# Optimization experiments

Measured on AMD Instinct MI355X. Metric: run time of the kernel, lower is better.

Reference implementation:

```python
import jax, jax.numpy as jnp
import numpy as np

B, C, H, W = 8, 384, 32, 32
KEYS, HEADS, U = 16, 4, 1
VS = C // HEADS
N = H * W
BN_EPS = 1e-5


def setup_inputs() -> dict:
    key = jax.random.key(0)
    ks = jax.random.split(key, 8)
    x = jax.random.normal(ks[0], (B, C, H, W), dtype=jnp.float32)
    # 1x1 convs (spectral-normalized in torch; SN only rescales the weight,
    # so a plain weight matrix computes the same functional form)
    Wq = jax.random.normal(ks[1], (KEYS * HEADS, C), dtype=jnp.float32) * 0.02
    Wk = jax.random.normal(ks[2], (KEYS * U, C), dtype=jnp.float32) * 0.02
    Wv = jax.random.normal(ks[3], (VS * U, C), dtype=jnp.float32) * 0.02
    # BatchNorm affine params (torch code xavier-inits weight, zeros bias)
    gamma_q = jax.random.normal(ks[4], (KEYS * HEADS,), dtype=jnp.float32)
    beta_q = jnp.zeros((KEYS * HEADS,), dtype=jnp.float32)
    gamma_v = jax.random.normal(ks[5], (VS * U,), dtype=jnp.float32)
    beta_v = jnp.zeros((VS * U,), dtype=jnp.float32)
    pos_emb = jax.random.normal(ks[6], (N, N, KEYS, U), dtype=jnp.float32)
    return {"x": x, "Wq": Wq, "Wk": Wk, "Wv": Wv,
            "gamma_q": gamma_q, "beta_q": beta_q,
            "gamma_v": gamma_v, "beta_v": beta_v,
            "pos_emb": pos_emb}


def _bn(z, gamma, beta):
    # z: (B, Ch, N); BatchNorm2d in training mode: biased batch stats over (B, N)
    mean = jnp.mean(z, axis=(0, 2), keepdims=True)
    var = jnp.var(z, axis=(0, 2), keepdims=True)
    zn = (z - mean) * jax.lax.rsqrt(var + BN_EPS)
    return zn * gamma[None, :, None] + beta[None, :, None]


def reference(x, Wq, Wk, Wv, gamma_q, beta_q, gamma_v, beta_v, pos_emb):
    xf = x.reshape(B, C, N)                       # 1x1 conv == per-pixel matmul
    q = jnp.einsum('oc,bcn->bon', Wq, xf)         # (B, KEYS*HEADS, N)
    k = jnp.einsum('oc,bcn->bon', Wk, xf)         # (B, KEYS*U, N)
    v = jnp.einsum('oc,bcn->bon', Wv, xf)         # (B, VS*U, N)
    q = _bn(q, gamma_q, beta_q)
    v = _bn(v, gamma_v, beta_v)
    q = q.reshape(B, HEADS, KEYS, N)
    k = k.reshape(B, U, KEYS, N)
    v = v.reshape(B, U, VS, N)
    k = jax.nn.softmax(k, axis=-1)
    lambdac = jnp.einsum('bukm,buvm->bkv', k, v)          # content lambda
    Yc = jnp.einsum('bhkn,bkv->bhvn', q, lambdac)
    lambdap = jnp.einsum('nmku,buvm->bnkv', pos_emb, v)   # position lambda (B,N,K,V)
    Yp = jnp.einsum('bhkn,bnkv->bhvn', q, lambdap)
    Y = (Yc + Yp).reshape(B, C, H, W)
    return Y
```

## Files before the change

kernel.cpp:

```cpp
#include <hip/hip_runtime.h>

typedef __attribute__((ext_vector_type(8))) short short8;
typedef __attribute__((ext_vector_type(16))) float floatx16;
typedef __attribute__((ext_vector_type(4))) float floatx4;
typedef unsigned short ushort16_t;
typedef unsigned int uint32;

#define BB 8
#define CC 384
#define NPIX 1024
#define TOTCH 176
#define BN_EPS 1e-5f

__device__ __forceinline__ ushort16_t f2bf(float x) {
    uint32 u = __float_as_uint(x);
    u += 0x7FFFu + ((u >> 16) & 1u);
    return (ushort16_t)(u >> 16);
}
__device__ __forceinline__ uint32 pk2(float a, float b) {
    uint32 ua = __float_as_uint(a); ua += 0x7FFFu + ((ua >> 16) & 1u);
    uint32 ub = __float_as_uint(b); ub += 0x7FFFu + ((ub >> 16) & 1u);
    return (ua >> 16) | (ub & 0xFFFF0000u);
}
__device__ __forceinline__ int div48(int x) {
    return (int)(((unsigned)x * 21846u) >> 20);
}
#define LGKM0_ONLY 0xC07F

__device__ __forceinline__ void gload8h(short8 &d, const ushort16_t* p) {
    asm volatile("global_load_dwordx4 %0, %1, off" : "=v"(d) : "v"(p));
}
__device__ __forceinline__ void gload4f(float4 &d, const float* p) {
    asm volatile("global_load_dwordx4 %0, %1, off" : "=v"(d) : "v"(p));
}


__global__ __launch_bounds__(256, 2) void k_wt(const float* __restrict__ Wq,
    const float* __restrict__ Wk, const float* __restrict__ Wv,
    ushort16_t* __restrict__ wbf)
{
    int bx = blockIdx.x, t = threadIdx.x;
    #pragma unroll
    for (int jj = 0; jj < 9; ++jj) {
        int idx8 = (bx * 9 + jj) * 256 + t;
        int row = div48(idx8);
        int g   = idx8 - row * 48;
        float4 f0, f1;
        if (row < 176) {
            const float* src;
            if (row < 64)       src = Wq + (size_t)row * CC;
            else if (row < 80)  src = Wk + (size_t)(row - 64) * CC;
            else                src = Wv + (size_t)(row - 80) * CC;
            f0 = *(const float4*)(src + g * 8);
            f1 = *(const float4*)(src + g * 8 + 4);
        } else {
            f0.x = f0.y = f0.z = f0.w = 0.f;
            f1 = f0;
        }
        uint4 w;
        w.x = pk2(f0.x, f0.y); w.y = pk2(f0.z, f0.w);
        w.z = pk2(f1.x, f1.y); w.w = pk2(f1.z, f1.w);
        *(uint4*)&wbf[(size_t)row * CC + g * 8] = w;
    }
}

__global__ __launch_bounds__(256, 2) void k_proj(const float* __restrict__ x,
    const ushort16_t* __restrict__ wbf, float* __restrict__ qkv)
{
    __shared__ __align__(16) ushort16_t XT[32 * 392];
    int bx = blockIdx.x, t = threadIdx.x;
    int b = bx >> 5, nbase = (bx & 31) * 32;
    const float* xb = x + (size_t)b * (CC * NPIX) + nbase;
    #pragma unroll
    for (int j = 0; j < 12; ++j) {
        int idx = t + 256 * j;
        int c = idx >> 3, ng = idx & 7;
        float4 f = *(const float4*)(xb + (size_t)c * NPIX + ng * 4);
        int col = ng * 4;
        XT[(col + 0) * 392 + c] = f2bf(f.x);
        XT[(col + 1) * 392 + c] = f2bf(f.y);
        XT[(col + 2) * 392 + c] = f2bf(f.z);
        XT[(col + 3) * 392 + c] = f2bf(f.w);
    }
    __syncthreads();

    int wave = t >> 6, lane = t & 63;
    int ct = wave & 1;
    int rs = wave >> 1;
    int col1 = lane & 15, kq = lane >> 4;
    const ushort16_t* bbase = &XT[(ct * 16 + col1) * 392 + kq * 8];
    int n = nbase + ct * 16 + col1;

    for (int r = rs; r < 11; r += 2) {
        int r0 = r * 16;
        const ushort16_t* ap = wbf + (size_t)(r0 + col1) * CC + kq * 8;
        floatx4 acc = {0.f, 0.f, 0.f, 0.f};
        short8 a0 = *(const short8*)ap;
        short8 b0 = *(const short8*)bbase;
        #pragma unroll
        for (int k = 1; k < 12; ++k) {
            short8 a1 = *(const short8*)(ap + k * 32);
            short8 b1 = *(const short8*)(bbase + k * 32);
            acc = __builtin_amdgcn_mfma_f32_16x16x32_bf16(a0, b0, acc, 0, 0, 0);
            a0 = a1; b0 = b1;
        }
        acc = __builtin_amdgcn_mfma_f32_16x16x32_bf16(a0, b0, acc, 0, 0, 0);
        #pragma unroll
        for (int rr = 0; rr < 4; ++rr) {
            int ch = r0 + kq * 4 + rr;
            qkv[((size_t)b * TOTCH + ch) * NPIX + n] = acc[rr];
        }
    }
}

__global__ __launch_bounds__(256, 2) void k_bnsm(const float* __restrict__ qkv,
    const float* __restrict__ gq, const float* __restrict__ bq,
    const float* __restrict__ gv, const float* __restrict__ bv,
    float* __restrict__ sA, float* __restrict__ sB, float* __restrict__ ksm)
{
    int bx = blockIdx.x, tid = threadIdx.x;
    int wid = tid >> 6, lane = tid & 63;
    if (bx < 160) {
        int ch = bx;
        int row; float gamma, beta;
        if (ch < 64) { row = ch; gamma = gq[ch]; beta = bq[ch]; }
        else { int j = ch - 64; row = 80 + j; gamma = gv[j]; beta = bv[j]; }
        float s = 0.f, ss = 0.f;
        #pragma unroll
        for (int j = 0; j < 8; ++j) {
            int i4 = tid + 256 * j;
            int b = i4 >> 8, n4 = i4 & 255;
            float4 f = *(const float4*)(qkv + ((size_t)b * TOTCH + row) * NPIX
                                            + n4 * 4);
            s  += f.x + f.y + f.z + f.w;
            ss += f.x * f.x + f.y * f.y + f.z * f.z + f.w * f.w;
        }
        #pragma unroll
        for (int off = 32; off > 0; off >>= 1) {
            s  += __shfl_down(s, off);
            ss += __shfl_down(ss, off);
        }
        __shared__ float rs[4], rss[4];
        if (lane == 0) { rs[wid] = s; rss[wid] = ss; }
        __syncthreads();
        if (tid == 0) {
            float S  = rs[0] + rs[1] + rs[2] + rs[3];
            float SS = rss[0] + rss[1] + rss[2] + rss[3];
            float inv = 1.f / (BB * NPIX);
            float mean = S * inv;
            float var  = SS * inv - mean * mean;
            float a = gamma * rsqrtf(var + BN_EPS);
            sA[row] = a;
            sB[row] = beta - mean * a;
        }
    } else {
        int idx = bx - 160;
        int kc = idx & 15, b = idx >> 4;
        const float* rowp = qkv + ((size_t)b * TOTCH + 64 + kc) * NPIX;
        float4 v4 = *(const float4*)(rowp + tid * 4);
        float v[4] = {v4.x, v4.y, v4.z, v4.w};
        float mx = fmaxf(fmaxf(v[0], v[1]), fmaxf(v[2], v[3]));
        #pragma unroll
        for (int off = 32; off > 0; off >>= 1) mx = fmaxf(mx, __shfl_down(mx, off));
        __shared__ float sm[4], ssum[4];
        if (lane == 0) sm[wid] = mx;
        __syncthreads();
        mx = fmaxf(fmaxf(sm[0], sm[1]), fmaxf(sm[2], sm[3]));
        float e[4], s = 0.f;
        #pragma unroll
        for (int j = 0; j < 4; ++j) { e[j] = __expf(v[j] - mx); s += e[j]; }
        #pragma unroll
        for (int off = 32; off > 0; off >>= 1) s += __shfl_down(s, off);
        if (lane == 0) ssum[wid] = s;
        __syncthreads();
        float inv = 1.f / (ssum[0] + ssum[1] + ssum[2] + ssum[3]);
        float4 o;
        o.x = e[0] * inv; o.y = e[1] * inv; o.z = e[2] * inv; o.w = e[3] * inv;
        *(float4*)(ksm + ((size_t)b * 16 + kc) * NPIX + tid * 4) = o;
    }
}

__global__ __launch_bounds__(256, 2) void k_packlc(const float* __restrict__ qkv,
    const float* __restrict__ sA, const float* __restrict__ sB,
    const float* __restrict__ ksm,
    ushort16_t* __restrict__ qt_g, ushort16_t* __restrict__ vt_g,
    ushort16_t* __restrict__ lc_g)
{
    int bx = blockIdx.x, t = threadIdx.x;
    if (bx < 128) {
        int bh = t & 31, nn = (t >> 5) & 7;
        int n = bx * 8 + nn;
        int b = bh >> 2, h = bh & 3;
        float vals[16];
        #pragma unroll
        for (int k = 0; k < 16; ++k) {
            int ch = h * 16 + k;
            vals[k] = qkv[((size_t)b * TOTCH + ch) * NPIX + n] * sA[ch] + sB[ch];
        }
        uint4 w0, w1;
        w0.x = pk2(vals[0], vals[1]);  w0.y = pk2(vals[2], vals[3]);
        w0.z = pk2(vals[4], vals[5]);  w0.w = pk2(vals[6], vals[7]);
        w1.x = pk2(vals[8], vals[9]);  w1.y = pk2(vals[10], vals[11]);
        w1.z = pk2(vals[12], vals[13]); w1.w = pk2(vals[14], vals[15]);
        *(uint4*)&qt_g[(size_t)n * 512 + bh * 8]       = w0;
        *(uint4*)&qt_g[(size_t)n * 512 + 256 + bh * 8] = w1;
    } else if (bx < 512) {
        int gi = (bx - 128) * 256 + t;
        int m8 = gi & 127;
        int vg = (gi >> 7) % 96;
        int b  = gi / (96 * 128);
        int m  = m8 * 8;
        int row = 80 + vg;
        float a = sA[row], bb = sB[row];
        const float* p = qkv + ((size_t)b * TOTCH + row) * NPIX + m;
        float4 f0 = *(const float4*)p;
        float4 f1 = *(const float4*)(p + 4);
        uint4 w;
        w.x = pk2(f0.x * a + bb, f0.y * a + bb);
        w.y = pk2(f0.z * a + bb, f0.w * a + bb);
        w.z = pk2(f1.x * a + bb, f1.y * a + bb);
        w.w = pk2(f1.z * a + bb, f1.w * a + bb);
        int mt = m >> 5, mq = (m >> 3) & 3;
        int vhh = vg / 48, vtt = (vg % 48) >> 4, vl = vg & 15;
        size_t idx = ((((size_t)b * 32 + mt) * 2 + vhh) * 3 + vtt) * 512
                   + mq * 128 + vl * 8;
        *(uint4*)&vt_g[idx] = w;
    } else {
        int gi = bx - 512;
        int v = gi % 96, b = gi / 96;
        int row = 80 + v;
        float a = sA[row], bb = sB[row];
        const float* vp = qkv + ((size_t)b * TOTCH + row) * NPIX;
        const float* kp = ksm + (size_t)b * 16 * NPIX;
        float4 vv = *(const float4*)(vp + t * 4);
        float4 vhat;
        vhat.x = vv.x * a + bb; vhat.y = vv.y * a + bb;
        vhat.z = vv.z * a + bb; vhat.w = vv.w * a + bb;
        float acc[16];
        #pragma unroll
        for (int k = 0; k < 16; ++k) {
            float4 kk = *(const float4*)(kp + (size_t)k * NPIX + t * 4);
            acc[k] = kk.x * vhat.x + kk.y * vhat.y
                   + kk.z * vhat.z + kk.w * vhat.w;
        }
        #pragma unroll
        for (int k = 0; k < 16; ++k) {
            #pragma unroll
            for (int off = 32; off > 0; off >>= 1)
                acc[k] += __shfl_down(acc[k], off);
        }
        __shared__ float red[16][4];
        int wid = t >> 6, lane = t & 63;
        if (lane == 0) {
            #pragma unroll
            for (int k = 0; k < 16; ++k) red[k][wid] = acc[k];
        }
        __syncthreads();
        int vhh = v / 48, vtt = (v % 48) >> 4, vl = v & 15;
        size_t plane = ((size_t)(b * 2 + vhh) * 3 + vtt) * 512;
        if (t < 16) {
            int k = t;
            float val = red[k][0] + red[k][1] + red[k][2] + red[k][3];
            lc_g[plane + (k >> 3) * 128 + vl * 8 + (k & 7)] = f2bf(val);
        } else if (t < 18) {
            int mq = 2 + (t - 16);
            uint4 z; z.x = z.y = z.z = z.w = 0u;
            *(uint4*)&lc_g[plane + mq * 128 + vl * 8] = z;
        }
    }
}

__global__ __attribute__((amdgpu_flat_work_group_size(512, 512)))
__attribute__((amdgpu_waves_per_eu(2, 2)))
void k_main(const float* __restrict__ pos,
    const ushort16_t* __restrict__ qt_g, const ushort16_t* __restrict__ vt_g,
    const ushort16_t* __restrict__ lc_g, float* __restrict__ out)
{
    __shared__ __align__(16) ushort16_t S_s[2][8256];
    int tid  = threadIdx.x;
    int lane = tid & 63;
    int wave = tid >> 6;
    int n0 = blockIdx.x * 4;

    int col1 = lane & 31, half = lane >> 5;
    int nsub = wave & 3, mc0 = wave >> 2;

    int colw  = (col1 & 3) * 4 + nsub;
    int key3w = nsub + ((col1 & 1) << 2);
    int basew = (col1 >> 2) * 1032 + colw * 64 + half * 4;

    int b2 = wave;
    int c2 = lane & 15, kq = lane >> 4;
    int h2 = c2 >> 2, n2 = c2 & 3;
    int key3r = n2 + ((h2 & 1) << 2);
    int baser = b2 * 1032 + (h2 * 4 + n2) * 64;

    short8 qfr = *(const short8*)(qt_g + (size_t)(n0 + nsub) * 512
                                  + half * 256 + col1 * 8);

    floatx4 acc[6];
    #pragma unroll
    for (int vg = 0; vg < 6; ++vg) acc[vg] = floatx4{0.f, 0.f, 0.f, 0.f};

    floatx16 z16;
    #pragma unroll
    for (int i = 0; i < 16; ++i) z16[i] = 0.f;

    const float* pA = pos + ((size_t)(n0 + nsub) * 1024 + mc0 * 32 + col1) * 16
                    + half * 8;
    const ushort16_t* pV = vt_g + (size_t)b2 * 98304 + lane * 8;

    float4 pa[2], pb[2];
    gload4f(pa[0], pA);
    gload4f(pb[0], pA + 4);
    gload4f(pa[1], pA + 1024);
    gload4f(pb[1], pA + 1028);

    short8 vbuf[12];

    #pragma unroll
    for (int i = 0; i < 16; ++i) {
        const ushort16_t* pVi = pV + (size_t)i * 6144;
        #pragma unroll
        for (int vg = 0; vg < 6; ++vg)
            gload8h(vbuf[vg], pVi + vg * 512);
        #pragma unroll
        for (int vg = 0; vg < 6; ++vg)
            gload8h(vbuf[6 + vg], pVi + 3072 + vg * 512);

        if (i == 0) {
            asm volatile("s_waitcnt vmcnt(14)");
            __builtin_amdgcn_sched_barrier(0);
        }

        {
            float4 a0c = pa[i & 1], a1c = pb[i & 1];
            uint4 aw;
            aw.x = pk2(a0c.x, a0c.y); aw.y = pk2(a0c.z, a0c.w);
            aw.z = pk2(a1c.x, a1c.y); aw.w = pk2(a1c.z, a1c.w);
            short8 afr = *(short8*)&aw;
            floatx16 d = __builtin_amdgcn_mfma_f32_32x32x16_bf16(
                afr, qfr, z16, 0, 0, 0);
            ushort16_t* Sb = S_s[i & 1];
            #pragma unroll
            for (int q = 0; q < 4; ++q) {
                int slot = (mc0 * 4 + q) ^ key3w;
                uint2 wv;
                wv.x = pk2(d[q * 4 + 0], d[q * 4 + 1]);
                wv.y = pk2(d[q * 4 + 2], d[q * 4 + 3]);
                *(uint2*)&Sb[basew + slot * 8] = wv;
            }
        }

        if (i < 14) {
            const float* p = pA + (size_t)(i + 2) * 1024;
            gload4f(pa[i & 1], p);
            gload4f(pb[i & 1], p + 4);
        }

        __builtin_amdgcn_s_waitcnt(LGKM0_ONLY);
        __builtin_amdgcn_s_barrier();

        if (i < 14) asm volatile("s_waitcnt vmcnt(2)");
        else        asm volatile("s_waitcnt vmcnt(0)");
        __builtin_amdgcn_sched_barrier(0);

        {
            const ushort16_t* Sr = S_s[i & 1];
            short8 bs0 = *(const short8*)&Sr[baser + (kq ^ key3r) * 8];
            #pragma unroll
            for (int vg = 0; vg < 6; ++vg)
                acc[vg] = __builtin_amdgcn_mfma_f32_16x16x32_bf16(
                    vbuf[vg], bs0, acc[vg], 0, 0, 0);
            short8 bs1 = *(const short8*)&Sr[baser + ((4 + kq) ^ key3r) * 8];
            #pragma unroll
            for (int vg = 0; vg < 6; ++vg)
                acc[vg] = __builtin_amdgcn_mfma_f32_16x16x32_bf16(
                    vbuf[6 + vg], bs1, acc[vg], 0, 0, 0);
        }
    }

    {
        short8 bsq = {0, 0, 0, 0, 0, 0, 0, 0};
        if (kq < 2)
            bsq = *(const short8*)(qt_g + (size_t)(n0 + n2) * 512
                                   + kq * 256 + (b2 * 4 + h2) * 8);
        const ushort16_t* lsrc = lc_g + (size_t)b2 * 3072 + lane * 8;
        #pragma unroll
        for (int vg = 0; vg < 6; ++vg) {
            short8 lv = *(const short8*)(lsrc + vg * 512);
            acc[vg] = __builtin_amdgcn_mfma_f32_16x16x32_bf16(
                lv, bsq, acc[vg], 0, 0, 0);
        }
    }

    {
        #pragma unroll
        for (int vg = 0; vg < 6; ++vg) {
            int vbase = (vg / 3) * 48 + (vg % 3) * 16 + kq * 4;
            #pragma unroll
            for (int r = 0; r < 4; ++r) {
                int v = vbase + r;
                out[(size_t)(b2 * 384 + h2 * 96 + v) * 1024 + n0 + n2]
                    = acc[vg][r];
            }
        }
    }
}

extern "C" void kernel_launch(void* const* d_in, const int* in_sizes, int n_in,
                              void* d_out, int out_size, void* d_ws, size_t ws_size,
                              hipStream_t stream) {
    const float* x   = (const float*)d_in[0];
    const float* Wq  = (const float*)d_in[1];
    const float* Wk  = (const float*)d_in[2];
    const float* Wv  = (const float*)d_in[3];
    const float* gq  = (const float*)d_in[4];
    const float* bq  = (const float*)d_in[5];
    const float* gv  = (const float*)d_in[6];
    const float* bv  = (const float*)d_in[7];
    const float* pos = (const float*)d_in[8];
    float* out = (float*)d_out;
    float* ws  = (float*)d_ws;

    float* qkv = ws;
    float* sA  = ws + 1441792;
    float* sB  = ws + 1441968;
    float* ksm = ws + 1442144;
    ushort16_t* qt_g = (ushort16_t*)(ws + 1573216);
    ushort16_t* vt_g = (ushort16_t*)(ws + 1835360);
    ushort16_t* lc_g = (ushort16_t*)(ws + 2228576);
    ushort16_t* wbf  = (ushort16_t*)(ws + 3813728);

    k_wt<<<dim3(4), dim3(256), 0, stream>>>(Wq, Wk, Wv, wbf);
    k_proj<<<dim3(256), dim3(256), 0, stream>>>(x, wbf, qkv);
    k_bnsm<<<dim3(288), dim3(256), 0, stream>>>(qkv, gq, bq, gv, bv, sA, sB, ksm);
    k_packlc<<<dim3(1280), dim3(256), 0, stream>>>(qkv, sA, sB, ksm,
                                                   qt_g, vt_g, lc_g);
    k_main<<<dim3(256), dim3(512), 0, stream>>>(pos, qt_g, vt_g, lc_g, out);
}
```

Measured before the change: 169.5 us.

## Stream V tiles through LDS with global_load_lds double buffering

Replaces the per-iteration register loads of twelve V fragments with direct global-to-LDS loads into two LDS half-buffers. Each half is refilled as soon as its MFMAs have consumed it, and the vmcnt waits are re-tuned to match. The pos-embedding prefetch distance drops from two iterations to one. The aim is to cut VGPR pressure and overlap V streaming with compute, at the cost of about 96KB of extra LDS, extra LDS reads, and tighter hand-managed wait counts.

New measurement: 174.3 us. 2.8% more time.

```diff
diff --git a/kernel.cpp b/kernel.cpp
--- a/kernel.cpp
+++ b/kernel.cpp
@@ -27,9 +27,6 @@
 }
 #define LGKM0_ONLY 0xC07F
 
-__device__ __forceinline__ void gload8h(short8 &d, const ushort16_t* p) {
-    asm volatile("global_load_dwordx4 %0, %1, off" : "=v"(d) : "v"(p));
-}
 __device__ __forceinline__ void gload4f(float4 &d, const float* p) {
     asm volatile("global_load_dwordx4 %0, %1, off" : "=v"(d) : "v"(p));
 }
@@ -277,6 +274,7 @@
     const ushort16_t* __restrict__ lc_g, float* __restrict__ out)
 {
     __shared__ __align__(16) ushort16_t S_s[2][8256];
+    __shared__ __align__(16) ushort16_t Vv[2][24576];
     int tid  = threadIdx.x;
     int lane = tid & 63;
     int wave = tid >> 6;
@@ -308,30 +306,37 @@
 
     const float* pA = pos + ((size_t)(n0 + nsub) * 1024 + mc0 * 32 + col1) * 16
                     + half * 8;
-    const ushort16_t* pV = vt_g + (size_t)b2 * 98304 + lane * 8;
+    const ushort16_t* vsrc = vt_g + (size_t)wave * 98304 + lane * 8;
 
     float4 pa[2], pb[2];
+
+    __builtin_amdgcn_sched_barrier(0);
     gload4f(pa[0], pA);
     gload4f(pb[0], pA + 4);
-    gload4f(pa[1], pA + 1024);
-    gload4f(pb[1], pA + 1028);
-
-    short8 vbuf[12];
+    #pragma unroll
+    for (int vg = 0; vg < 6; ++vg)
+        __builtin_amdgcn_global_load_lds(
+            (const uint4*)(vsrc + vg * 512),
+            (uint4*)&Vv[0][wave * 3072 + vg * 512], 16, 0, 0);
+    #pragma unroll
+    for (int vg = 0; vg < 6; ++vg)
+        __builtin_amdgcn_global_load_lds(
+            (const uint4*)(vsrc + 3072 + vg * 512),
+            (uint4*)&Vv[1][wave * 3072 + vg * 512], 16, 0, 0);
+    __builtin_amdgcn_sched_barrier(0);
 
     #pragma unroll
     for (int i = 0; i < 16; ++i) {
-        const ushort16_t* pVi = pV + (size_t)i * 6144;
-        #pragma unroll
-        for (int vg = 0; vg < 6; ++vg)
-            gload8h(vbuf[vg], pVi + vg * 512);
-        #pragma unroll
-        for (int vg = 0; vg < 6; ++vg)
-            gload8h(vbuf[6 + vg], pVi + 3072 + vg * 512);
-
-        if (i == 0) {
+        if (i < 15) {
+            const float* p = pA + (size_t)(i + 1) * 1024;
+            __builtin_amdgcn_sched_barrier(0);
+            gload4f(pa[(i + 1) & 1], p);
+            gload4f(pb[(i + 1) & 1], p + 4);
             asm volatile("s_waitcnt vmcnt(14)");
-            __builtin_amdgcn_sched_barrier(0);
-        }
+        } else {
+            asm volatile("s_waitcnt vmcnt(12)");
+        }
+        __builtin_amdgcn_sched_barrier(0);
 
         {
             float4 a0c = pa[i & 1], a1c = pb[i & 1];
@@ -352,31 +357,55 @@
             }
         }
 
-        if (i < 14) {
-            const float* p = pA + (size_t)(i + 2) * 1024;
-            gload4f(pa[i & 1], p);
-            gload4f(pb[i & 1], p + 4);
-        }
-
         __builtin_amdgcn_s_waitcnt(LGKM0_ONLY);
         __builtin_amdgcn_s_barrier();
 
-        if (i < 14) asm volatile("s_waitcnt vmcnt(2)");
+        if (i < 15) asm volatile("s_waitcnt vmcnt(8)");
+        else        asm volatile("s_waitcnt vmcnt(6)");
+        __builtin_amdgcn_sched_barrier(0);
+        {
+            const ushort16_t* Sr = S_s[i & 1];
+            const ushort16_t* Vr0 = &Vv[0][b2 * 3072 + lane * 8];
+            short8 bs0 = *(const short8*)&Sr[baser + (kq ^ key3r) * 8];
+            #pragma unroll
+            for (int vg = 0; vg < 6; ++vg)
+                acc[vg] = __builtin_amdgcn_mfma_f32_16x16x32_bf16(
+                    *(const short8*)(Vr0 + vg * 512), bs0, acc[vg], 0, 0, 0);
+        }
+        if (i < 15) {
+            asm volatile("s_waitcnt lgkmcnt(0)");
+            __builtin_amdgcn_sched_barrier(0);
+            const ushort16_t* vs = vsrc + (size_t)(2 * i + 2) * 3072;
+            #pragma unroll
+            for (int vg = 0; vg < 6; ++vg)
+                __builtin_amdgcn_global_load_lds(
+                    (const uint4*)(vs + vg * 512),
+                    (uint4*)&Vv[0][wave * 3072 + vg * 512], 16, 0, 0);
+            __builtin_amdgcn_sched_barrier(0);
+        }
+
+        if (i < 15) asm volatile("s_waitcnt vmcnt(8)");
         else        asm volatile("s_waitcnt vmcnt(0)");
         __builtin_amdgcn_sched_barrier(0);
-
         {
             const ushort16_t* Sr = S_s[i & 1];
-            short8 bs0 = *(const short8*)&Sr[baser + (kq ^ key3r) * 8];
+            const ushort16_t* Vr1 = &Vv[1][b2 * 3072 + lane * 8];
+            short8 bs1 = *(const short8*)&Sr[baser + ((4 + kq) ^ key3r) * 8];
             #pragma unroll
             for (int vg = 0; vg < 6; ++vg)
                 acc[vg] = __builtin_amdgcn_mfma_f32_16x16x32_bf16(
-                    vbuf[vg], bs0, acc[vg], 0, 0, 0);
-            short8 bs1 = *(const short8*)&Sr[baser + ((4 + kq) ^ key3r) * 8];
+                    *(const short8*)(Vr1 + vg * 512), bs1, acc[vg], 0, 0, 0);
+        }
+        if (i < 15) {
+            asm volatile("s_waitcnt lgkmcnt(0)");
+            __builtin_amdgcn_sched_barrier(0);
+            const ushort16_t* vs = vsrc + (size_t)(2 * i + 3) * 3072;
             #pragma unroll
             for (int vg = 0; vg < 6; ++vg)
-                acc[vg] = __builtin_amdgcn_mfma_f32_16x16x32_bf16(
-                    vbuf[6 + vg], bs1, acc[vg], 0, 0, 0);
+                __builtin_amdgcn_global_load_lds(
+                    (const uint4*)(vs + vg * 512),
+                    (uint4*)&Vv[1][wave * 3072 + vg * 512], 16, 0, 0);
+            __builtin_amdgcn_sched_barrier(0);
         }
     }
 
```

## Retile main kernel to 16 pixels per block with LDS-staged V and split-M atomics

Applied to the files above, without the earlier changes.

The main kernel now handles 16 output pixels per block instead of 4. It splits the value channels into halves and the m (key position) range into halves across a 3D grid. V tiles are staged into LDS with global_load_lds and double buffered, so each V load is reused across four pixel groups instead of being reloaded into registers per pixel. Partial results from the two m halves are combined with atomic adds, which needs a new zeroing kernel on the output. This adds an extra launch plus atomic traffic, and makes the summation order nondeterministic.

After: 233.1 us. +37.5%, slower.

```diff
diff --git a/kernel.cpp b/kernel.cpp
--- a/kernel.cpp
+++ b/kernel.cpp
@@ -27,13 +27,19 @@
 }
 #define LGKM0_ONLY 0xC07F
 
-__device__ __forceinline__ void gload8h(short8 &d, const ushort16_t* p) {
-    asm volatile("global_load_dwordx4 %0, %1, off" : "=v"(d) : "v"(p));
-}
 __device__ __forceinline__ void gload4f(float4 &d, const float* p) {
     asm volatile("global_load_dwordx4 %0, %1, off" : "=v"(d) : "v"(p));
 }
 
+
+__global__ __launch_bounds__(256) void k_zero(float* __restrict__ out)
+{
+    int i = blockIdx.x * 256 + threadIdx.x;
+    float4 z; z.x = z.y = z.z = z.w = 0.f;
+    #pragma unroll
+    for (int j = 0; j < 4; ++j)
+        *(float4*)(out + (size_t)(i + j * 196608) * 4) = z;
+}
 
 __global__ __launch_bounds__(256, 2) void k_wt(const float* __restrict__ Wq,
     const float* __restrict__ Wk, const float* __restrict__ Wv,
@@ -277,10 +283,13 @@
     const ushort16_t* __restrict__ lc_g, float* __restrict__ out)
 {
     __shared__ __align__(16) ushort16_t S_s[2][8256];
+    __shared__ __align__(16) ushort16_t Vv[2][24576];
     int tid  = threadIdx.x;
     int lane = tid & 63;
     int wave = tid >> 6;
-    int n0 = blockIdx.x * 4;
+    int n0 = blockIdx.x * 16;
+    int vh = blockIdx.y;
+    int mz = blockIdx.z;
 
     int col1 = lane & 31, half = lane >> 5;
     int nsub = wave & 3, mc0 = wave >> 2;
@@ -295,53 +304,80 @@
     int key3r = n2 + ((h2 & 1) << 2);
     int baser = b2 * 1032 + (h2 * 4 + n2) * 64;
 
-    short8 qfr = *(const short8*)(qt_g + (size_t)(n0 + nsub) * 512
-                                  + half * 256 + col1 * 8);
-
-    floatx4 acc[6];
-    #pragma unroll
-    for (int vg = 0; vg < 6; ++vg) acc[vg] = floatx4{0.f, 0.f, 0.f, 0.f};
+    short8 qfr[4];
+    #pragma unroll
+    for (int ng = 0; ng < 4; ++ng)
+        qfr[ng] = *(const short8*)(qt_g + (size_t)(n0 + ng * 4 + nsub) * 512
+                                   + half * 256 + col1 * 8);
+
+    floatx4 acc[4][3];
+    #pragma unroll
+    for (int ng = 0; ng < 4; ++ng)
+        #pragma unroll
+        for (int vt = 0; vt < 3; ++vt)
+            acc[ng][vt] = floatx4{0.f, 0.f, 0.f, 0.f};
 
     floatx16 z16;
     #pragma unroll
     for (int i = 0; i < 16; ++i) z16[i] = 0.f;
 
-    const float* pA = pos + ((size_t)(n0 + nsub) * 1024 + mc0 * 32 + col1) * 16
-                    + half * 8;
-    const ushort16_t* pV = vt_g + (size_t)b2 * 98304 + lane * 8;
+    const float* pA = pos + ((size_t)(n0 + nsub) * 1024 + mz * 512
+                             + mc0 * 32 + col1) * 16 + half * 8;
+    const ushort16_t* vsrc = vt_g + ((size_t)wave * 32 + mz * 16) * 3072
+                           + (size_t)vh * 1536 + lane * 8;
 
     float4 pa[2], pb[2];
+
+    __builtin_amdgcn_sched_barrier(0);
     gload4f(pa[0], pA);
     gload4f(pb[0], pA + 4);
-    gload4f(pa[1], pA + 1024);
-    gload4f(pb[1], pA + 1028);
-
-    short8 vbuf[12];
-
-    #pragma unroll
-    for (int i = 0; i < 16; ++i) {
-        const ushort16_t* pVi = pV + (size_t)i * 6144;
-        #pragma unroll
-        for (int vg = 0; vg < 6; ++vg)
-            gload8h(vbuf[vg], pVi + vg * 512);
-        #pragma unroll
-        for (int vg = 0; vg < 6; ++vg)
-            gload8h(vbuf[6 + vg], pVi + 3072 + vg * 512);
-
-        if (i == 0) {
-            asm volatile("s_waitcnt vmcnt(14)");
+    #pragma unroll
+    for (int mc = 0; mc < 2; ++mc)
+        #pragma unroll
+        for (int vt = 0; vt < 3; ++vt)
+            __builtin_amdgcn_global_load_lds(
+                (const uint4*)(vsrc + mc * 3072 + vt * 512),
+                (uint4*)&Vv[0][wave * 3072 + mc * 1536 + vt * 512], 16, 0, 0);
+    __builtin_amdgcn_sched_barrier(0);
+
+    #pragma unroll
+    for (int s = 0; s < 32; ++s) {
+        const int mi = s >> 2, ng = s & 3;
+        if (s < 31) {
+            const int mi1 = (s + 1) >> 2, ng1 = (s + 1) & 3;
+            const float* p = pA + (size_t)ng1 * 65536 + mi1 * 1024;
             __builtin_amdgcn_sched_barrier(0);
-        }
+            gload4f(pa[(s + 1) & 1], p);
+            gload4f(pb[(s + 1) & 1], p + 4);
+        }
+        if (ng == 0 && mi < 7) {
+            asm volatile("s_waitcnt lgkmcnt(0)");
+            __builtin_amdgcn_sched_barrier(0);
+            const ushort16_t* vs = vsrc + (size_t)((mi + 1) * 2) * 3072;
+            #pragma unroll
+            for (int mc = 0; mc < 2; ++mc)
+                #pragma unroll
+                for (int vt = 0; vt < 3; ++vt)
+                    __builtin_amdgcn_global_load_lds(
+                        (const uint4*)(vs + mc * 3072 + vt * 512),
+                        (uint4*)&Vv[(mi + 1) & 1][wave * 3072 + mc * 1536
+                                                  + vt * 512], 16, 0, 0);
+        }
+        if (s == 31)                    asm volatile("s_waitcnt vmcnt(0)");
+        else if (ng <= 1 && mi < 7)     asm volatile("s_waitcnt vmcnt(8)");
+        else if (ng <= 1 && mi == 7 && s > 0) asm volatile("s_waitcnt vmcnt(2)");
+        else                            asm volatile("s_waitcnt vmcnt(2)");
+        __builtin_amdgcn_sched_barrier(0);
 
         {
-            float4 a0c = pa[i & 1], a1c = pb[i & 1];
+            float4 a0c = pa[s & 1], a1c = pb[s & 1];
             uint4 aw;
             aw.x = pk2(a0c.x, a0c.y); aw.y = pk2(a0c.z, a0c.w);
             aw.z = pk2(a1c.x, a1c.y); aw.w = pk2(a1c.z, a1c.w);
             short8 afr = *(short8*)&aw;
             floatx16 d = __builtin_amdgcn_mfma_f32_32x32x16_bf16(
-                afr, qfr, z16, 0, 0, 0);
-            ushort16_t* Sb = S_s[i & 1];
+                afr, qfr[ng], z16, 0, 0, 0);
+            ushort16_t* Sb = S_s[s & 1];
             #pragma unroll
             for (int q = 0; q < 4; ++q) {
                 int slot = (mc0 * 4 + q) ^ key3w;
@@ -352,57 +388,58 @@
             }
         }
 
-        if (i < 14) {
-            const float* p = pA + (size_t)(i + 2) * 1024;
-            gload4f(pa[i & 1], p);
-            gload4f(pb[i & 1], p + 4);
-        }
-
         __builtin_amdgcn_s_waitcnt(LGKM0_ONLY);
         __builtin_amdgcn_s_barrier();
 
-        if (i < 14) asm volatile("s_waitcnt vmcnt(2)");
-        else        asm volatile("s_waitcnt vmcnt(0)");
-        __builtin_amdgcn_sched_barrier(0);
-
         {
-            const ushort16_t* Sr = S_s[i & 1];
+            const ushort16_t* Sr = S_s[s & 1];
+            const ushort16_t* Vp = &Vv[mi & 1][b2 * 3072 + lane * 8];
             short8 bs0 = *(const short8*)&Sr[baser + (kq ^ key3r) * 8];
             #pragma unroll
-            for (int vg = 0; vg < 6; ++vg)
-                acc[vg] = __builtin_amdgcn_mfma_f32_16x16x32_bf16(
-                    vbuf[vg], bs0, acc[vg], 0, 0, 0);
+            for (int vt = 0; vt < 3; ++vt)
+                acc[ng][vt] = __builtin_amdgcn_mfma_f32_16x16x32_bf16(
+                    *(const short8*)(Vp + vt * 512), bs0, acc[ng][vt], 0, 0, 0);
             short8 bs1 = *(const short8*)&Sr[baser + ((4 + kq) ^ key3r) * 8];
             #pragma unroll
-            for (int vg = 0; vg < 6; ++vg)
-                acc[vg] = __builtin_amdgcn_mfma_f32_16x16x32_bf16(
-                    vbuf[6 + vg], bs1, acc[vg], 0, 0, 0);
+            for (int vt = 0; vt < 3; ++vt)
+                acc[ng][vt] = __builtin_amdgcn_mfma_f32_16x16x32_bf16(
+                    *(const short8*)(Vp + 1536 + vt * 512), bs1,
+                    acc[ng][vt], 0, 0, 0);
+        }
+    }
+
+    if (mz == 0) {
+        const ushort16_t* lsrc = lc_g + ((size_t)b2 * 2 + vh) * 1536 + lane * 8;
+        short8 lv[3];
+        #pragma unroll
+        for (int vt = 0; vt < 3; ++vt)
+            lv[vt] = *(const short8*)(lsrc + vt * 512);
+        #pragma unroll
+        for (int ng = 0; ng < 4; ++ng) {
+            short8 bsq = {0, 0, 0, 0, 0, 0, 0, 0};
+            if (kq < 2)
+                bsq = *(const short8*)(qt_g + (size_t)(n0 + ng * 4 + n2) * 512
+                                       + kq * 256 + (b2 * 4 + h2) * 8);
+            #pragma unroll
+            for (int vt = 0; vt < 3; ++vt)
+                acc[ng][vt] = __builtin_amdgcn_mfma_f32_16x16x32_bf16(
+                    lv[vt], bsq, acc[ng][vt], 0, 0, 0);
         }
     }
 
     {
-        short8 bsq = {0, 0, 0, 0, 0, 0, 0, 0};
-        if (kq < 2)
-            bsq = *(const short8*)(qt_g + (size_t)(n0 + n2) * 512
-                                   + kq * 256 + (b2 * 4 + h2) * 8);
-        const ushort16_t* lsrc = lc_g + (size_t)b2 * 3072 + lane * 8;
-        #pragma unroll
-        for (int vg = 0; vg < 6; ++vg) {
-            short8 lv = *(const short8*)(lsrc + vg * 512);
-            acc[vg] = __builtin_amdgcn_mfma_f32_16x16x32_bf16(
-                lv, bsq, acc[vg], 0, 0, 0);
-        }
-    }
-
-    {
-        #pragma unroll
-        for (int vg = 0; vg < 6; ++vg) {
-            int vbase = (vg / 3) * 48 + (vg % 3) * 16 + kq * 4;
-            #pragma unroll
-            for (int r = 0; r < 4; ++r) {
-                int v = vbase + r;
-                out[(size_t)(b2 * 384 + h2 * 96 + v) * 1024 + n0 + n2]
-                    = acc[vg][r];
+        #pragma unroll
+        for (int ng = 0; ng < 4; ++ng) {
+            #pragma unroll
+            for (int vt = 0; vt < 3; ++vt) {
+                #pragma unroll
+                for (int r = 0; r < 4; ++r) {
+                    int v = vh * 48 + vt * 16 + kq * 4 + r;
+                    unsafeAtomicAdd(
+                        &out[(size_t)(b2 * 384 + h2 * 96 + v) * 1024
+                             + n0 + ng * 4 + n2],
+                        acc[ng][vt][r]);
+                }
             }
         }
     }
@@ -432,10 +469,11 @@
     ushort16_t* lc_g = (ushort16_t*)(ws + 2228576);
     ushort16_t* wbf  = (ushort16_t*)(ws + 3813728);
 
+    k_zero<<<dim3(768), dim3(256), 0, stream>>>(out);
     k_wt<<<dim3(4), dim3(256), 0, stream>>>(Wq, Wk, Wv, wbf);
     k_proj<<<dim3(256), dim3(256), 0, stream>>>(x, wbf, qkv);
     k_bnsm<<<dim3(288), dim3(256), 0, stream>>>(qkv, gq, bq, gv, bv, sA, sB, ksm);
     k_packlc<<<dim3(1280), dim3(256), 0, stream>>>(qkv, sA, sB, ksm,
                                                    qt_g, vt_g, lc_g);
-    k_main<<<dim3(256), dim3(512), 0, stream>>>(pos, qt_g, vt_g, lc_g, out);
-}
+    k_main<<<dim3(64, 2, 2), dim3(512), 0, stream>>>(pos, qt_g, vt_g, lc_g, out);
+}
```
